# Optimization experiments

Hardware: AMD Instinct MI355X
Metric: run time of the kernel (lower is better)

## Reference

```python
import jax, jax.numpy as jnp
import numpy as np

N, D, H, E = 50000, 128, 128, 800000


def setup_inputs() -> dict:
    key = jax.random.key(0)
    ks = jax.random.split(key, 12)
    p = lambda k, shape: jax.random.normal(k, shape, dtype=jnp.float32) * 0.02
    z = lambda n: jnp.zeros((n,), jnp.float32)
    return {
        "x1": jax.random.normal(ks[0], (N, D), dtype=jnp.float32),
        "edge_index1": jax.random.randint(ks[1], (2, E), 0, N, dtype=jnp.int32),
        "x2": jax.random.normal(ks[2], (N, D), dtype=jnp.float32),
        "edge_index2": jax.random.randint(ks[3], (2, E), 0, N, dtype=jnp.int32),
        "enc_w1": p(ks[4], (D, H)), "enc_b1": z(H),
        "enc_w2": p(ks[5], (H, H)), "enc_b2": z(H),
        "conv1_w": p(ks[6], (H, H)), "conv1_b": z(H),
        "conv2_w": p(ks[7], (H, H)), "conv2_b": z(H),
        "sim_w1": p(ks[8], (4 * H, H)), "sim_b1": z(H),
        "sim_w2": p(ks[9], (H, 1)), "sim_b2": z(1),
    }


def reference(x1, edge_index1, x2, edge_index2,
              enc_w1, enc_b1, enc_w2, enc_b2,
              conv1_w, conv1_b, conv2_w, conv2_b,
              sim_w1, sim_b1, sim_w2, sim_b2):
    def gcn(x, ei, W, b):
        row, col = ei[0], ei[1]            # [E], [E]
        h = x @ W + b                      # [N, H]
        n = x.shape[0]
        deg = jax.ops.segment_sum(jnp.ones(row.shape[0], h.dtype), row, num_segments=n)
        dis = jnp.where(deg > 0, deg ** -0.5, 0.0)   # deg^-0.5, inf -> 0
        norm = dis[row] * dis[col]         # [E]
        msg = h[col] * norm[:, None]       # gather + per-edge scale, [E, H]
        return jax.ops.segment_sum(msg, row, num_segments=n)  # scatter-add

    def embed(x, ei):
        h = jax.nn.relu(x @ enc_w1 + enc_b1) @ enc_w2 + enc_b2  # encoder MLP
        h = jax.nn.relu(gcn(h, ei, conv1_w, conv1_b))
        h = jax.nn.relu(gcn(h, ei, conv2_w, conv2_b))
        return h.mean(axis=0)              # mean pooling -> [H]

    g1 = embed(x1, edge_index1)
    g2 = embed(x2, edge_index2)
    c = jnp.concatenate([g1, g2, jnp.abs(g1 - g2), g1 * g2], axis=-1)  # [4H]
    return jax.nn.relu(c @ sim_w1 + sim_b1) @ sim_w2 + sim_b2          # [1]
```

## Files before the change

### kernel.cpp

```cpp
#include <hip/hip_runtime.h>

#define HD 128

typedef _Float16 f16x8 __attribute__((ext_vector_type(8)));
typedef _Float16 f16x2 __attribute__((ext_vector_type(2)));
typedef float f32x4 __attribute__((ext_vector_type(4)));

template<bool RELU, bool SCALE, bool CVT, bool WF16>
__device__ __forceinline__ void gemm_block(
    _Float16* lds, int bi,
    const _Float16* __restrict__ Ab, const float* __restrict__ Af0,
    const float* __restrict__ Af1, const void* __restrict__ Wsrc,
    const float* __restrict__ bias, const float* __restrict__ scale,
    _Float16* __restrict__ C, int N, int Ntot) {
  const int tid = threadIdx.x;
  if (WF16) {
    const _Float16* Wf = (const _Float16*)Wsrc;
    #pragma unroll
    for (int i = 0; i < 8; ++i)
      *(float4*)&lds[tid * 8 + i * 2048] = *(const float4*)&Wf[tid * 8 + i * 2048];
  } else {
    const float* Wg = (const float*)Wsrc;
    #pragma unroll
    for (int i = 0; i < 16; ++i) {
      int flat = i * 1024 + tid * 4;
      int k = flat >> 7, n0 = flat & 127;
      float4 w4 = *(const float4*)(Wg + flat);
      int kc = k >> 5, q = (k >> 3) & 3, j = k & 7;
      float wv[4] = {w4.x, w4.y, w4.z, w4.w};
      #pragma unroll
      for (int d = 0; d < 4; ++d) {
        int n = n0 + d;
        lds[(size_t)(((n >> 4) * 4 + kc) * 64 + 16 * q + (n & 15)) * 8 + j] = (_Float16)wv[d];
      }
    }
  }
  __syncthreads();

  const int lane = tid & 63;
  const int wave = tid >> 6;
  const int n16 = lane & 15, q = lane >> 4;
  const int rowbase = bi * 128 + wave * 32;

  int arow[2];
  #pragma unroll
  for (int t = 0; t < 2; ++t) {
    int r = rowbase + 16 * t + n16;
    arow[t] = (r < Ntot) ? r : (Ntot - 1);
  }

  f32x4 acc[2][8];
  #pragma unroll
  for (int t = 0; t < 2; ++t)
    #pragma unroll
    for (int nt = 0; nt < 8; ++nt) acc[t][nt] = (f32x4){0.f, 0.f, 0.f, 0.f};

  #pragma unroll
  for (int kc = 0; kc < 4; ++kc) {
    f16x8 a[2];
    #pragma unroll
    for (int t = 0; t < 2; ++t) {
      if (CVT) {
        int r = arow[t];
        const float* src = (r < N) ? (Af0 + (size_t)r * HD) : (Af1 + (size_t)(r - N) * HD);
        float4 u0 = *(const float4*)(src + kc * 32 + q * 8);
        float4 u1 = *(const float4*)(src + kc * 32 + q * 8 + 4);
        union { _Float16 h[8]; f16x8 v; } tmp;
        tmp.h[0] = (_Float16)u0.x; tmp.h[1] = (_Float16)u0.y;
        tmp.h[2] = (_Float16)u0.z; tmp.h[3] = (_Float16)u0.w;
        tmp.h[4] = (_Float16)u1.x; tmp.h[5] = (_Float16)u1.y;
        tmp.h[6] = (_Float16)u1.z; tmp.h[7] = (_Float16)u1.w;
        a[t] = tmp.v;
      } else {
        a[t] = *(const f16x8*)(Ab + (size_t)arow[t] * HD + kc * 32 + q * 8);
      }
    }
    #pragma unroll
    for (int nt = 0; nt < 8; ++nt) {
      f16x8 b = *(const f16x8*)&lds[(size_t)((nt * 4 + kc) * 64 + lane) * 8];
      #pragma unroll
      for (int t = 0; t < 2; ++t)
        acc[t][nt] = __builtin_amdgcn_mfma_f32_16x16x32_f16(a[t], b, acc[t][nt], 0, 0, 0);
    }
  }

  float bv[8];
  #pragma unroll
  for (int nt = 0; nt < 8; ++nt) bv[nt] = bias[nt * 16 + n16];

  #pragma unroll
  for (int t = 0; t < 2; ++t) {
    #pragma unroll
    for (int r = 0; r < 4; ++r) {
      int row = rowbase + 16 * t + 4 * q + r;
      if (row < Ntot) {
        float s = SCALE ? scale[row] : 1.0f;
        #pragma unroll
        for (int nt = 0; nt < 8; ++nt) {
          float v = acc[t][nt][r] + bv[nt];
          if (RELU) v = fmaxf(v, 0.f);
          if (SCALE) v *= s;
          C[(size_t)row * HD + nt * 16 + n16] = (_Float16)v;
        }
      }
    }
  }
}

template<bool RELU, bool SCALE, bool CVT, bool WF16, int AUX>
__global__ __launch_bounds__(256, 4) void k_fused(
    const _Float16* __restrict__ Ab, const float* __restrict__ Af0,
    const float* __restrict__ Af1, const void* __restrict__ Wsrc,
    const float* __restrict__ bias, const float* __restrict__ scale,
    _Float16* __restrict__ C, int N, int Ntot, int auxN,
    const int* __restrict__ ei0, const int* __restrict__ ei1, int E,
    int* __restrict__ deg2, unsigned short* __restrict__ slot,
    const float* __restrict__ w1, const float* __restrict__ w2,
    const float* __restrict__ w3, _Float16* __restrict__ WfOut, int degB,
    int* __restrict__ offs, int* __restrict__ partials,
    float* __restrict__ dis, int scanBlocks) {
  __shared__ _Float16 lds[16384];
  const int bi = blockIdx.x;
  const int t = threadIdx.x;
  if (bi >= auxN) {
    gemm_block<RELU, SCALE, CVT, WF16>(lds, bi - auxN, Ab, Af0, Af1, Wsrc,
                                       bias, scale, C, N, Ntot);
    return;
  }
  if (AUX == 1) {
    if (bi < 2 * degB) {
      int g = (bi >= degB);
      int cb = bi - g * degB;
      const int* rows = g ? ei1 : ei0;
      int* deg = deg2 + g * N;
      unsigned short* sl = slot + (size_t)g * E;
      int base = (cb * 256 + t) * 4;
      if (base + 3 < E) {
        int4 r = *(const int4*)(rows + base);
        union { unsigned short us[4]; uint2 v; } s;
        s.us[0] = (unsigned short)atomicAdd(&deg[r.x], 1);
        s.us[1] = (unsigned short)atomicAdd(&deg[r.y], 1);
        s.us[2] = (unsigned short)atomicAdd(&deg[r.z], 1);
        s.us[3] = (unsigned short)atomicAdd(&deg[r.w], 1);
        *(uint2*)(sl + base) = s.v;
      } else {
        for (int e = base; e < E; ++e)
          sl[e] = (unsigned short)atomicAdd(&deg[rows[e]], 1);
      }
    } else {
      int wb = bi - 2 * degB;
      int m = wb >> 3;
      const float* Wg = (m == 0) ? w1 : (m == 1) ? w2 : w3;
      int idx0 = (wb & 7) * 2048 + t * 8;
      float4 u0 = *(const float4*)(Wg + idx0);
      float4 u1 = *(const float4*)(Wg + idx0 + 4);
      int k = idx0 >> 7, n0 = idx0 & 127;
      int kc = k >> 5, q2 = (k >> 3) & 3, j = k & 7;
      _Float16* dst = WfOut + (size_t)m * 16384;
      float vv[8] = {u0.x, u0.y, u0.z, u0.w, u1.x, u1.y, u1.z, u1.w};
      #pragma unroll
      for (int d = 0; d < 8; ++d) {
        int n = n0 + d;
        dst[(size_t)(((n >> 4) * 4 + kc) * 64 + 16 * q2 + (n & 15)) * 8 + j] = (_Float16)vv[d];
      }
    }
  } else if (AUX == 2) {
    int* s = (int*)lds;
    int i = bi * 256 + t;
    int v = (i < Ntot) ? deg2[i] : 0;
    s[t] = v;
    __syncthreads();
    #pragma unroll
    for (int off = 1; off < 256; off <<= 1) {
      int x = (t >= off) ? s[t - off] : 0;
      __syncthreads();
      s[t] += x;
      __syncthreads();
    }
    if (i < Ntot) {
      offs[i] = s[t] - v;
      dis[i] = (v > 0) ? (1.0f / sqrtf((float)v)) : 0.0f;
    }
    if (t == 255) partials[bi] = s[255];
  } else if (AUX == 3) {
    int* s = (int*)lds;
    int P = scanBlocks;
    int v0 = (t < P) ? partials[t] : 0;
    int v1 = (t + 256 < P) ? partials[t + 256] : 0;
    s[t] = v0;
    s[t + 256] = v1;
    __syncthreads();
    #pragma unroll
    for (int off = 1; off < 256; off <<= 1) {
      int x0 = (t >= off) ? s[t - off] : 0;
      int x1 = (t >= off) ? s[256 + t - off] : 0;
      __syncthreads();
      s[t] += x0;
      s[256 + t] += x1;
      __syncthreads();
    }
    int tot0 = s[255];
    if (t < P) partials[t] = s[t] - v0;
    if (t + 256 < P) partials[t + 256] = s[256 + t] + tot0 - v1;
  }
}

__global__ void k_csr_fill(const int* __restrict__ ei0, const int* __restrict__ ei1,
                           int E, int N, const int* __restrict__ offs,
                           const int* __restrict__ partials,
                           const unsigned short* __restrict__ slot,
                           unsigned short* __restrict__ csr_col) {
  int g = blockIdx.y;
  const int* eg = (g ? ei1 : ei0);
  const int* ob = offs + g * N;
  const int* pb = partials;
  const unsigned short* sl = slot + (size_t)g * E;
  int gN = g * N;
  int base = (blockIdx.x * 256 + threadIdx.x) * 4;
  if (base + 3 < E) {
    int4 r = *(const int4*)(eg + base);
    int4 c = *(const int4*)(eg + E + base);
    uint2 sv = *(const uint2*)(sl + base);
    csr_col[ob[r.x] + pb[(gN + r.x) >> 8] + (sv.x & 0xffff)] = (unsigned short)c.x;
    csr_col[ob[r.y] + pb[(gN + r.y) >> 8] + (sv.x >> 16)]    = (unsigned short)c.y;
    csr_col[ob[r.z] + pb[(gN + r.z) >> 8] + (sv.y & 0xffff)] = (unsigned short)c.z;
    csr_col[ob[r.w] + pb[(gN + r.w) >> 8] + (sv.y >> 16)]    = (unsigned short)c.w;
  } else {
    for (int e = base; e < E; ++e)
      csr_col[ob[eg[e]] + pb[(gN + eg[e]) >> 8] + sl[e]] = (unsigned short)eg[E + e];
  }
}

template<bool POOL>
__global__ __launch_bounds__(256) void k_aggregate(
    const _Float16* __restrict__ T, const int* __restrict__ offs,
    const int* __restrict__ partials, const unsigned short* __restrict__ csr_col,
    const float* __restrict__ dis, _Float16* __restrict__ out,
    float* __restrict__ poolrep, int N, int Ntot, int Etot) {
  __shared__ float red[4][128];
  const int lane = threadIdx.x & 63;
  const int wave = threadIdx.x >> 6;
  const int gw = blockIdx.x * 4 + wave;
  const int sub = lane >> 4, c16 = lane & 15;

  f16x2 hacc[4];
  #pragma unroll
  for (int j = 0; j < 4; ++j) hacc[j] = (f16x2){(_Float16)0.f, (_Float16)0.f};

  if (gw < Ntot) {
    const int beg = offs[gw] + partials[gw >> 8];
    const int end = (gw + 1 == Ntot) ? Etot : (offs[gw + 1] + partials[(gw + 1) >> 8]);
    const uint4* Tg = (const uint4*)(T + (size_t)(gw >= N ? N : 0) * HD);
    for (int e = beg; e < end; e += 16) {
      uint4 v[4];
      #pragma unroll
      for (int gp = 0; gp < 4; ++gp) {
        v[gp] = make_uint4(0, 0, 0, 0);
        if (e + 4 * gp < end) {
          int eg = e + 4 * gp + sub;
          bool valid = (eg < end);
          int ce = valid ? eg : (end - 1);
          int col = csr_col[ce];
          uint4 tv = Tg[(size_t)col * 16 + c16];
          if (valid) v[gp] = tv;
        }
      }
      #pragma unroll
      for (int gp = 0; gp < 4; ++gp) {
        union { uint4 u; f16x2 h[4]; } w;
        w.u = v[gp];
        hacc[0] += w.h[0];
        hacc[1] += w.h[1];
        hacc[2] += w.h[2];
        hacc[3] += w.h[3];
      }
    }
  }

  float ax[8];
  #pragma unroll
  for (int j = 0; j < 4; ++j) {
    ax[2 * j]     = (float)hacc[j][0];
    ax[2 * j + 1] = (float)hacc[j][1];
  }
  #pragma unroll
  for (int j = 0; j < 8; ++j) {
    ax[j] += __shfl_xor(ax[j], 32, 64);
    ax[j] += __shfl_xor(ax[j], 16, 64);
  }
  float dr = (gw < Ntot) ? dis[gw] : 0.f;
  #pragma unroll
  for (int j = 0; j < 8; ++j) ax[j] = fmaxf(ax[j] * dr, 0.f);

  if (!POOL) {
    if (gw < Ntot && sub == 0) {
      union { uint4 u; _Float16 h[8]; } o;
      #pragma unroll
      for (int j = 0; j < 8; ++j) o.h[j] = (_Float16)ax[j];
      ((uint4*)out)[(size_t)gw * 16 + c16] = o.u;
    }
  } else {
    if (sub == 0) {
      *(float4*)&red[wave][c16 * 8]     = make_float4(ax[0], ax[1], ax[2], ax[3]);
      *(float4*)&red[wave][c16 * 8 + 4] = make_float4(ax[4], ax[5], ax[6], ax[7]);
    }
    __syncthreads();
    int t = threadIdx.x;
    if (t < 128) {
      float s = red[0][t] + red[1][t] + red[2][t] + red[3][t];
      int g = (blockIdx.x * 4 >= N) ? 1 : 0;
      atomicAdd(&poolrep[(size_t)((blockIdx.x & 15) * 2 + g) * 128 + t], s);
    }
  }
}

__global__ void k_final(const float* __restrict__ poolrep,
                        const float* __restrict__ W1, const float* __restrict__ b1,
                        const float* __restrict__ W2, const float* __restrict__ b2,
                        float* __restrict__ out, float invN) {
  __shared__ float cs[512];
  __shared__ float red[2];
  int t = threadIdx.x;
  float g1 = 0.f, g2 = 0.f;
  #pragma unroll
  for (int r = 0; r < 16; ++r) {
    g1 += poolrep[r * 256 + t];
    g2 += poolrep[r * 256 + 128 + t];
  }
  g1 *= invN;
  g2 *= invN;
  cs[t] = g1;
  cs[128 + t] = g2;
  cs[256 + t] = fabsf(g1 - g2);
  cs[384 + t] = g1 * g2;
  __syncthreads();
  float acc = b1[t];
  #pragma unroll 8
  for (int i = 0; i < 512; ++i) acc = fmaf(cs[i], W1[(size_t)i * HD + t], acc);
  float h = fmaxf(acc, 0.f);
  float v = h * W2[t];
  #pragma unroll
  for (int off = 32; off > 0; off >>= 1) v += __shfl_down(v, off, 64);
  if ((t & 63) == 0) red[t >> 6] = v;
  __syncthreads();
  if (t == 0) out[0] = red[0] + red[1] + b2[0];
}

extern "C" void kernel_launch(void* const* d_in, const int* in_sizes, int n_in,
                              void* d_out, int out_size, void* d_ws, size_t ws_size,
                              hipStream_t stream) {
  const float* x1     = (const float*)d_in[0];
  const int*   ei1    = (const int*)d_in[1];
  const float* x2     = (const float*)d_in[2];
  const int*   ei2    = (const int*)d_in[3];
  const float* W_in[4] = {(const float*)d_in[4], (const float*)d_in[6],
                          (const float*)d_in[8], (const float*)d_in[10]};
  const float* B_in[4] = {(const float*)d_in[5], (const float*)d_in[7],
                          (const float*)d_in[9], (const float*)d_in[11]};
  const float* sim_w1 = (const float*)d_in[12];
  const float* sim_b1 = (const float*)d_in[13];
  const float* sim_w2 = (const float*)d_in[14];
  const float* sim_b2 = (const float*)d_in[15];

  const int N = in_sizes[0] / HD;
  const int E = in_sizes[1] / 2;
  const int Ntot = 2 * N;

  _Float16* sp = (_Float16*)d_ws;
  _Float16* bufA = sp; sp += (size_t)Ntot * HD;
  _Float16* bufB = sp; sp += (size_t)Ntot * HD;
  _Float16* WfB  = sp; sp += 3 * 16384;
  float* fp = (float*)sp;
  float* dis     = fp; fp += Ntot;
  float* poolrep = fp; fp += 16 * 256;
  int* ip = (int*)fp;
  int* deg2     = ip; ip += Ntot;
  int* offs     = ip; ip += Ntot;
  int* partials = ip; ip += 512;
  ip = (int*)(((uintptr_t)ip + 15) & ~(uintptr_t)15);
  unsigned short* slot = (unsigned short*)ip;
  unsigned short* csr_col = slot + 2 * (size_t)E;

  const int G = (Ntot + 127) / 128;
  const int scanB = (Ntot + 255) / 256;
  const int aggB  = (Ntot + 3) / 4;
  const int degB  = (E + 1023) / 1024;
  const dim3 fillGrid(((E + 3) / 4 + 255) / 256, 2);

  hipMemsetAsync(poolrep, 0, (16 * 256 + Ntot) * sizeof(float), stream);

  {
    int auxN = 2 * degB + 24;
    k_fused<true, false, true, false, 1><<<auxN + G, 256, 0, stream>>>(
        nullptr, x1, x2, W_in[0], B_in[0], nullptr, bufA, N, Ntot, auxN,
        ei1, ei2, E, deg2, slot, W_in[1], W_in[2], W_in[3], WfB, degB,
        offs, partials, dis, scanB);
  }
  k_fused<false, false, false, true, 2><<<scanB + G, 256, 0, stream>>>(
      bufA, nullptr, nullptr, WfB + 0 * 16384, B_in[1], nullptr, bufB, N, Ntot, scanB,
      nullptr, nullptr, E, deg2, nullptr, nullptr, nullptr, nullptr, nullptr, degB,
      offs, partials, dis, scanB);
  k_fused<false, true, false, true, 3><<<1 + G, 256, 0, stream>>>(
      bufB, nullptr, nullptr, WfB + 1 * 16384, B_in[2], dis, bufA, N, Ntot, 1,
      nullptr, nullptr, E, deg2, nullptr, nullptr, nullptr, nullptr, nullptr, degB,
      offs, partials, dis, scanB);
  k_csr_fill<<<fillGrid, 256, 0, stream>>>(ei1, ei2, E, N, offs, partials, slot, csr_col);
  k_aggregate<false><<<aggB, 256, 0, stream>>>(bufA, offs, partials, csr_col, dis,
                                               bufB, nullptr, N, Ntot, 2 * E);
  k_fused<false, true, false, true, 0><<<G, 256, 0, stream>>>(
      bufB, nullptr, nullptr, WfB + 2 * 16384, B_in[3], dis, bufA, N, Ntot, 0,
      nullptr, nullptr, E, deg2, nullptr, nullptr, nullptr, nullptr, nullptr, degB,
      offs, partials, dis, scanB);
  k_aggregate<true><<<aggB, 256, 0, stream>>>(bufA, offs, partials, csr_col, dis,
                                              nullptr, poolrep, N, Ntot, 2 * E);
  k_final<<<1, 128, 0, stream>>>(poolrep, sim_w1, sim_b1, sim_w2, sim_b2,
                                 (float*)d_out, 1.0f / (float)N);
}
```

Measured before the change: 418.8 us.

## Fold scan finalize, CSR fill and final MLP into existing kernels via last-block counters

```diff
diff --git a/kernel.cpp b/kernel.cpp
--- a/kernel.cpp
+++ b/kernel.cpp
@@ -107,30 +107,46 @@
   }
 }
 
-template<bool RELU, bool SCALE, bool CVT, bool WF16, int AUX>
+template<bool RELU, bool SCALE, bool CVT, bool WF16, int AUX, int PAT>
 __global__ __launch_bounds__(256, 4) void k_fused(
     const _Float16* __restrict__ Ab, const float* __restrict__ Af0,
     const float* __restrict__ Af1, const void* __restrict__ Wsrc,
     const float* __restrict__ bias, const float* __restrict__ scale,
-    _Float16* __restrict__ C, int N, int Ntot, int auxN,
+    _Float16* __restrict__ C, int N, int Ntot, int G, int A,
     const int* __restrict__ ei0, const int* __restrict__ ei1, int E,
     int* __restrict__ deg2, unsigned short* __restrict__ slot,
     const float* __restrict__ w1, const float* __restrict__ w2,
     const float* __restrict__ w3, _Float16* __restrict__ WfOut, int degB,
     int* __restrict__ offs, int* __restrict__ partials,
-    float* __restrict__ dis, int scanBlocks) {
+    float* __restrict__ dis, int scanB,
+    unsigned short* __restrict__ csr_col, int fillB, int* __restrict__ ctr) {
   __shared__ _Float16 lds[16384];
+  __shared__ int lastFlag;
   const int bi = blockIdx.x;
   const int t = threadIdx.x;
-  if (bi >= auxN) {
-    gemm_block<RELU, SCALE, CVT, WF16>(lds, bi - auxN, Ab, Af0, Af1, Wsrc,
+
+  int role, rid;
+  if (PAT == 2) { role = 0; rid = bi; }
+  else if (PAT == 0) {
+    if (bi < 3 * G) { int k = bi / 3, r = bi % 3;
+      if (r == 2) { role = 0; rid = k; } else { role = 1; rid = 2 * k + r; } }
+    else { role = 1; rid = bi - G; }
+  } else {
+    if (bi < 3 * A) { int k = bi / 3, r = bi % 3;
+      if (r == 2) { role = 1; rid = k; } else { role = 0; rid = 2 * k + r; } }
+    else { role = 0; rid = bi - A; }
+  }
+
+  if (role == 0) {
+    gemm_block<RELU, SCALE, CVT, WF16>(lds, rid, Ab, Af0, Af1, Wsrc,
                                        bias, scale, C, N, Ntot);
     return;
   }
+
   if (AUX == 1) {
-    if (bi < 2 * degB) {
-      int g = (bi >= degB);
-      int cb = bi - g * degB;
+    if (rid < 2 * degB) {
+      int g = (rid >= degB);
+      int cb = rid - g * degB;
       const int* rows = g ? ei1 : ei0;
       int* deg = deg2 + g * N;
       unsigned short* sl = slot + (size_t)g * E;
@@ -148,7 +164,7 @@
           sl[e] = (unsigned short)atomicAdd(&deg[rows[e]], 1);
       }
     } else {
-      int wb = bi - 2 * degB;
+      int wb = rid - 2 * degB;
       int m = wb >> 3;
       const float* Wg = (m == 0) ? w1 : (m == 1) ? w2 : w3;
       int idx0 = (wb & 7) * 2048 + t * 8;
@@ -166,7 +182,7 @@
     }
   } else if (AUX == 2) {
     int* s = (int*)lds;
-    int i = bi * 256 + t;
+    int i = rid * 256 + t;
     int v = (i < Ntot) ? deg2[i] : 0;
     s[t] = v;
     __syncthreads();
@@ -181,53 +197,56 @@
       offs[i] = s[t] - v;
       dis[i] = (v > 0) ? (1.0f / sqrtf((float)v)) : 0.0f;
     }
-    if (t == 255) partials[bi] = s[255];
-  } else if (AUX == 3) {
-    int* s = (int*)lds;
-    int P = scanBlocks;
-    int v0 = (t < P) ? partials[t] : 0;
-    int v1 = (t + 256 < P) ? partials[t + 256] : 0;
-    s[t] = v0;
-    s[t + 256] = v1;
+    if (t == 255) partials[rid] = s[255];
     __syncthreads();
-    #pragma unroll
-    for (int off = 1; off < 256; off <<= 1) {
-      int x0 = (t >= off) ? s[t - off] : 0;
-      int x1 = (t >= off) ? s[256 + t - off] : 0;
+    if (t == 0) {
+      __threadfence();
+      lastFlag = (atomicAdd(ctr, 1) == scanB - 1);
+    }
+    __syncthreads();
+    if (lastFlag) {
+      __threadfence();
+      volatile int* vp = partials;
+      int P = scanB;
+      int v0 = (t < P) ? vp[t] : 0;
+      int v1 = (t + 256 < P) ? vp[t + 256] : 0;
       __syncthreads();
-      s[t] += x0;
-      s[256 + t] += x1;
+      s[t] = v0;
+      s[t + 256] = v1;
       __syncthreads();
-    }
-    int tot0 = s[255];
-    if (t < P) partials[t] = s[t] - v0;
-    if (t + 256 < P) partials[t + 256] = s[256 + t] + tot0 - v1;
-  }
-}
-
-__global__ void k_csr_fill(const int* __restrict__ ei0, const int* __restrict__ ei1,
-                           int E, int N, const int* __restrict__ offs,
-                           const int* __restrict__ partials,
-                           const unsigned short* __restrict__ slot,
-                           unsigned short* __restrict__ csr_col) {
-  int g = blockIdx.y;
-  const int* eg = (g ? ei1 : ei0);
-  const int* ob = offs + g * N;
-  const int* pb = partials;
-  const unsigned short* sl = slot + (size_t)g * E;
-  int gN = g * N;
-  int base = (blockIdx.x * 256 + threadIdx.x) * 4;
-  if (base + 3 < E) {
-    int4 r = *(const int4*)(eg + base);
-    int4 c = *(const int4*)(eg + E + base);
-    uint2 sv = *(const uint2*)(sl + base);
-    csr_col[ob[r.x] + pb[(gN + r.x) >> 8] + (sv.x & 0xffff)] = (unsigned short)c.x;
-    csr_col[ob[r.y] + pb[(gN + r.y) >> 8] + (sv.x >> 16)]    = (unsigned short)c.y;
-    csr_col[ob[r.z] + pb[(gN + r.z) >> 8] + (sv.y & 0xffff)] = (unsigned short)c.z;
-    csr_col[ob[r.w] + pb[(gN + r.w) >> 8] + (sv.y >> 16)]    = (unsigned short)c.w;
-  } else {
-    for (int e = base; e < E; ++e)
-      csr_col[ob[eg[e]] + pb[(gN + eg[e]) >> 8] + sl[e]] = (unsigned short)eg[E + e];
+      #pragma unroll
+      for (int off = 1; off < 256; off <<= 1) {
+        int x0 = (t >= off) ? s[t - off] : 0;
+        int x1 = (t >= off) ? s[256 + t - off] : 0;
+        __syncthreads();
+        s[t] += x0;
+        s[256 + t] += x1;
+        __syncthreads();
+      }
+      int tot0 = s[255];
+      if (t < P) partials[t] = s[t] - v0;
+      if (t + 256 < P) partials[t + 256] = s[256 + t] + tot0 - v1;
+    }
+  } else if (AUX == 4) {
+    int g = (rid >= fillB);
+    int cb = rid - g * fillB;
+    const int* eg = (g ? ei1 : ei0);
+    const int* ob = offs + g * N;
+    const unsigned short* sl = slot + (size_t)g * E;
+    int gN = g * N;
+    int base = (cb * 256 + t) * 4;
+    if (base + 3 < E) {
+      int4 r = *(const int4*)(eg + base);
+      int4 c = *(const int4*)(eg + E + base);
+      uint2 sv = *(const uint2*)(sl + base);
+      csr_col[ob[r.x] + partials[(gN + r.x) >> 8] + (sv.x & 0xffff)] = (unsigned short)c.x;
+      csr_col[ob[r.y] + partials[(gN + r.y) >> 8] + (sv.x >> 16)]    = (unsigned short)c.y;
+      csr_col[ob[r.z] + partials[(gN + r.z) >> 8] + (sv.y & 0xffff)] = (unsigned short)c.z;
+      csr_col[ob[r.w] + partials[(gN + r.w) >> 8] + (sv.y >> 16)]    = (unsigned short)c.w;
+    } else {
+      for (int e = base; e < E; ++e)
+        csr_col[ob[eg[e]] + partials[(gN + eg[e]) >> 8] + sl[e]] = (unsigned short)eg[E + e];
+    }
   }
 }
 
@@ -236,8 +255,12 @@
     const _Float16* __restrict__ T, const int* __restrict__ offs,
     const int* __restrict__ partials, const unsigned short* __restrict__ csr_col,
     const float* __restrict__ dis, _Float16* __restrict__ out,
-    float* __restrict__ poolrep, int N, int Ntot, int Etot) {
+    float* __restrict__ poolrep, int N, int Ntot, int Etot,
+    const float* __restrict__ W1, const float* __restrict__ b1,
+    const float* __restrict__ W2, const float* __restrict__ b2,
+    float* __restrict__ result, float invN, int* __restrict__ ctr, int nBlocks) {
   __shared__ float red[4][128];
+  __shared__ int lastFlag;
   const int lane = threadIdx.x & 63;
   const int wave = threadIdx.x >> 6;
   const int gw = blockIdx.x * 4 + wave;
@@ -299,51 +322,58 @@
       for (int j = 0; j < 8; ++j) o.h[j] = (_Float16)ax[j];
       ((uint4*)out)[(size_t)gw * 16 + c16] = o.u;
     }
-  } else {
-    if (sub == 0) {
-      *(float4*)&red[wave][c16 * 8]     = make_float4(ax[0], ax[1], ax[2], ax[3]);
-      *(float4*)&red[wave][c16 * 8 + 4] = make_float4(ax[4], ax[5], ax[6], ax[7]);
-    }
-    __syncthreads();
-    int t = threadIdx.x;
-    if (t < 128) {
-      float s = red[0][t] + red[1][t] + red[2][t] + red[3][t];
-      int g = (blockIdx.x * 4 >= N) ? 1 : 0;
-      atomicAdd(&poolrep[(size_t)((blockIdx.x & 15) * 2 + g) * 128 + t], s);
-    }
-  }
-}
-
-__global__ void k_final(const float* __restrict__ poolrep,
-                        const float* __restrict__ W1, const float* __restrict__ b1,
-                        const float* __restrict__ W2, const float* __restrict__ b2,
-                        float* __restrict__ out, float invN) {
+    return;
+  }
+
+  if (sub == 0) {
+    *(float4*)&red[wave][c16 * 8]     = make_float4(ax[0], ax[1], ax[2], ax[3]);
+    *(float4*)&red[wave][c16 * 8 + 4] = make_float4(ax[4], ax[5], ax[6], ax[7]);
+  }
+  __syncthreads();
+  int t = threadIdx.x;
+  if (t < 128) {
+    float s = red[0][t] + red[1][t] + red[2][t] + red[3][t];
+    int g = (blockIdx.x * 4 >= N) ? 1 : 0;
+    atomicAdd(&poolrep[(size_t)((blockIdx.x & 15) * 2 + g) * 128 + t], s);
+  }
+  __syncthreads();
+  if (t == 0) {
+    __threadfence();
+    lastFlag = (atomicAdd(ctr, 1) == nBlocks - 1);
+  }
+  __syncthreads();
+  if (!lastFlag) return;
+
+  __threadfence();
   __shared__ float cs[512];
-  __shared__ float red[2];
-  int t = threadIdx.x;
+  __shared__ float red2[2];
   float g1 = 0.f, g2 = 0.f;
-  #pragma unroll
-  for (int r = 0; r < 16; ++r) {
-    g1 += poolrep[r * 256 + t];
-    g2 += poolrep[r * 256 + 128 + t];
-  }
-  g1 *= invN;
-  g2 *= invN;
-  cs[t] = g1;
-  cs[128 + t] = g2;
-  cs[256 + t] = fabsf(g1 - g2);
-  cs[384 + t] = g1 * g2;
-  __syncthreads();
-  float acc = b1[t];
-  #pragma unroll 8
-  for (int i = 0; i < 512; ++i) acc = fmaf(cs[i], W1[(size_t)i * HD + t], acc);
-  float h = fmaxf(acc, 0.f);
-  float v = h * W2[t];
-  #pragma unroll
-  for (int off = 32; off > 0; off >>= 1) v += __shfl_down(v, off, 64);
-  if ((t & 63) == 0) red[t >> 6] = v;
-  __syncthreads();
-  if (t == 0) out[0] = red[0] + red[1] + b2[0];
+  if (t < 128) {
+    #pragma unroll
+    for (int r = 0; r < 16; ++r) {
+      g1 += *(volatile float*)&poolrep[r * 256 + t];
+      g2 += *(volatile float*)&poolrep[r * 256 + 128 + t];
+    }
+    g1 *= invN;
+    g2 *= invN;
+    cs[t] = g1;
+    cs[128 + t] = g2;
+    cs[256 + t] = fabsf(g1 - g2);
+    cs[384 + t] = g1 * g2;
+  }
+  __syncthreads();
+  if (t < 128) {
+    float acc = b1[t];
+    #pragma unroll 8
+    for (int i = 0; i < 512; ++i) acc = fmaf(cs[i], W1[(size_t)i * HD + t], acc);
+    float h = fmaxf(acc, 0.f);
+    float v = h * W2[t];
+    #pragma unroll
+    for (int off = 32; off > 0; off >>= 1) v += __shfl_down(v, off, 64);
+    if ((t & 63) == 0) red2[t >> 6] = v;
+  }
+  __syncthreads();
+  if (t == 0) result[0] = red2[0] + red2[1] + b2[0];
 }
 
 extern "C" void kernel_launch(void* const* d_in, const int* in_sizes, int n_in,
@@ -374,6 +404,7 @@
   float* dis     = fp; fp += Ntot;
   float* poolrep = fp; fp += 16 * 256;
   int* ip = (int*)fp;
+  int* ctrs     = ip; ip += 8;
   int* deg2     = ip; ip += Ntot;
   int* offs     = ip; ip += Ntot;
   int* partials = ip; ip += 512;
@@ -384,35 +415,34 @@
   const int G = (Ntot + 127) / 128;
   const int scanB = (Ntot + 255) / 256;
   const int aggB  = (Ntot + 3) / 4;
-  const int degB  = (E + 1023) / 1024;
-  const dim3 fillGrid(((E + 3) / 4 + 255) / 256, 2);
-
-  hipMemsetAsync(poolrep, 0, (16 * 256 + Ntot) * sizeof(float), stream);
+  const int degB  = ((E + 3) / 4 + 255) / 256;
+  const int fillB = degB;
+
+  hipMemsetAsync(poolrep, 0, (16 * 256 + 8 + Ntot) * sizeof(float), stream);
 
   {
-    int auxN = 2 * degB + 24;
-    k_fused<true, false, true, false, 1><<<auxN + G, 256, 0, stream>>>(
-        nullptr, x1, x2, W_in[0], B_in[0], nullptr, bufA, N, Ntot, auxN,
+    int A = 2 * degB + 24;
+    k_fused<true, false, true, false, 1, 0><<<A + G, 256, 0, stream>>>(
+        nullptr, x1, x2, W_in[0], B_in[0], nullptr, bufA, N, Ntot, G, A,
         ei1, ei2, E, deg2, slot, W_in[1], W_in[2], W_in[3], WfB, degB,
-        offs, partials, dis, scanB);
-  }
-  k_fused<false, false, false, true, 2><<<scanB + G, 256, 0, stream>>>(
-      bufA, nullptr, nullptr, WfB + 0 * 16384, B_in[1], nullptr, bufB, N, Ntot, scanB,
-      nullptr, nullptr, E, deg2, nullptr, nullptr, nullptr, nullptr, nullptr, degB,
-      offs, partials, dis, scanB);
-  k_fused<false, true, false, true, 3><<<1 + G, 256, 0, stream>>>(
-      bufB, nullptr, nullptr, WfB + 1 * 16384, B_in[2], dis, bufA, N, Ntot, 1,
-      nullptr, nullptr, E, deg2, nullptr, nullptr, nullptr, nullptr, nullptr, degB,
-      offs, partials, dis, scanB);
-  k_csr_fill<<<fillGrid, 256, 0, stream>>>(ei1, ei2, E, N, offs, partials, slot, csr_col);
-  k_aggregate<false><<<aggB, 256, 0, stream>>>(bufA, offs, partials, csr_col, dis,
-                                               bufB, nullptr, N, Ntot, 2 * E);
-  k_fused<false, true, false, true, 0><<<G, 256, 0, stream>>>(
-      bufB, nullptr, nullptr, WfB + 2 * 16384, B_in[3], dis, bufA, N, Ntot, 0,
-      nullptr, nullptr, E, deg2, nullptr, nullptr, nullptr, nullptr, nullptr, degB,
-      offs, partials, dis, scanB);
-  k_aggregate<true><<<aggB, 256, 0, stream>>>(bufA, offs, partials, csr_col, dis,
-                                              nullptr, poolrep, N, Ntot, 2 * E);
-  k_final<<<1, 128, 0, stream>>>(poolrep, sim_w1, sim_b1, sim_w2, sim_b2,
-                                 (float*)d_out, 1.0f / (float)N);
+        offs, partials, dis, scanB, csr_col, fillB, ctrs);
+  }
+  k_fused<false, false, false, true, 2, 1><<<scanB + G, 256, 0, stream>>>(
+      bufA, nullptr, nullptr, WfB + 0 * 16384, B_in[1], nullptr, bufB, N, Ntot, G, scanB,
+      ei1, ei2, E, deg2, slot, nullptr, nullptr, nullptr, nullptr, degB,
+      offs, partials, dis, scanB, csr_col, fillB, ctrs);
+  k_fused<false, true, false, true, 4, 0><<<2 * fillB + G, 256, 0, stream>>>(
+      bufB, nullptr, nullptr, WfB + 1 * 16384, B_in[2], dis, bufA, N, Ntot, G, 2 * fillB,
+      ei1, ei2, E, deg2, slot, nullptr, nullptr, nullptr, nullptr, degB,
+      offs, partials, dis, scanB, csr_col, fillB, ctrs);
+  k_aggregate<false><<<aggB, 256, 0, stream>>>(
+      bufA, offs, partials, csr_col, dis, bufB, nullptr, N, Ntot, 2 * E,
+      nullptr, nullptr, nullptr, nullptr, nullptr, 0.f, nullptr, 0);
+  k_fused<false, true, false, true, 0, 2><<<G, 256, 0, stream>>>(
+      bufB, nullptr, nullptr, WfB + 2 * 16384, B_in[3], dis, bufA, N, Ntot, G, 0,
+      ei1, ei2, E, deg2, slot, nullptr, nullptr, nullptr, nullptr, degB,
+      offs, partials, dis, scanB, csr_col, fillB, ctrs);
+  k_aggregate<true><<<aggB, 256, 0, stream>>>(
+      bufA, offs, partials, csr_col, dis, nullptr, poolrep, N, Ntot, 2 * E,
+      sim_w1, sim_b1, sim_w2, sim_b2, (float*)d_out, 1.0f / (float)N, ctrs + 1, aggB);
 }
```

New measurement: 1.080 ms. 158% more time.
